# Kernel tuning notes

Hardware: AMD Instinct MI355X
Metric: run time of the kernel (lower is better)

Reference implementation:

```python
import jax, jax.numpy as jnp
import numpy as np

B, S, E, C, H = 64, 2048, 512, 512, 256


def setup_inputs() -> dict:
    key = jax.random.key(0)
    ks = jax.random.split(key, 8)
    encoder_word_embeds = jax.random.normal(ks[0], (B, S, E), dtype=jnp.float32)
    encoder_lengths = jax.random.randint(ks[1], (B,), 1, S + 1)  # lengths in [1, S]
    context_state = jax.random.normal(ks[2], (B, C), dtype=jnp.float32)
    # Learned parameters (nn.Linear style: y = x @ W.T + b)
    sw = 1.0 / np.sqrt(E)
    sc = 1.0 / np.sqrt(C)
    sh = 1.0 / np.sqrt(H)
    W_word = jax.random.uniform(ks[3], (H, E), minval=-sw, maxval=sw, dtype=jnp.float32)
    b_word = jax.random.uniform(ks[4], (H,), minval=-sw, maxval=sw, dtype=jnp.float32)
    W_ctx = jax.random.uniform(ks[5], (H, C), minval=-sc, maxval=sc, dtype=jnp.float32)
    b_ctx = jax.random.uniform(ks[6], (H,), minval=-sc, maxval=sc, dtype=jnp.float32)
    w_hidden = jax.random.uniform(ks[7], (H,), minval=-sh, maxval=sh, dtype=jnp.float32)  # hidden_layer has no bias
    return {
        "encoder_word_embeds": encoder_word_embeds,
        "encoder_lengths": encoder_lengths,
        "context_state": context_state,
        "W_word": W_word,
        "b_word": b_word,
        "W_ctx": W_ctx,
        "b_ctx": b_ctx,
        "w_hidden": w_hidden,
    }


def reference(encoder_word_embeds, encoder_lengths, context_state, W_word, b_word, W_ctx, b_ctx, w_hidden):
    seq_len = encoder_word_embeds.shape[1]
    # word mask [B, S]: positions < length
    positions = jnp.arange(seq_len)  # [S]
    mask = (positions[None, :] < encoder_lengths[:, None]).astype(jnp.float32)  # [B, S]
    # additive attention MLP
    word_feat = jnp.einsum("bse,he->bsh", encoder_word_embeds, W_word) + b_word  # [B,S,H]
    ctx_feat = context_state @ W_ctx.T + b_ctx  # [B,H]
    scores = jnp.einsum("bsh,h->bs", jnp.tanh(word_feat + ctx_feat[:, None, :]), w_hidden)  # [B,S]
    # softmax over seq, then mask and renormalize (matches original order)
    attn = jax.nn.softmax(scores, axis=1) * mask
    attn = attn / (1e-10 + attn.sum(axis=1, keepdims=True))  # [B,S]
    attention_features = jnp.einsum("bs,bse->be", attn, encoder_word_embeds)  # [B,E]
    return attention_features, attn
```

## Files before the change

kernel.cpp:

```cpp
#include <hip/hip_runtime.h>
#include <hip/hip_bf16.h>
#include <cstdint>
#include <cstddef>

#define B_  64
#define S_  2048
#define E_  512
#define C_  512
#define H_  256

using f32x4 = __attribute__((ext_vector_type(4))) float;
using s16x8 = __attribute__((ext_vector_type(8))) short;

__device__ __forceinline__ uint2 f4_to_bf4(float4 v) {
    __hip_bfloat162 lo = __float22bfloat162_rn(make_float2(v.x, v.y));
    __hip_bfloat162 hi = __float22bfloat162_rn(make_float2(v.z, v.w));
    union { __hip_bfloat162 b; unsigned u; } a, c;
    a.b = lo; c.b = hi;
    return make_uint2(a.u, c.u);
}

__global__ void prep_w(const float* __restrict__ W, unsigned short* __restrict__ Wb) {
    int i = (blockIdx.x * 256 + threadIdx.x) * 4;
    float4 v = *(const float4*)(W + i);
    uint2 o = f4_to_bf4(v);
    *(uint2*)(Wb + i) = o;
}

__global__ void prep_ctx(const float* __restrict__ ctx, const float* __restrict__ Wc,
                         const float* __restrict__ bc, const float* __restrict__ bw,
                         float* __restrict__ cb) {
    __shared__ float row[C_];
    int b = blockIdx.x, t = threadIdx.x;
    row[t] = ctx[b * C_ + t];
    row[t + 256] = ctx[b * C_ + t + 256];
    __syncthreads();
    const float4* w4 = (const float4*)(Wc + (size_t)t * C_);
    const float4* x4 = (const float4*)row;
    float acc = 0.f;
    #pragma unroll 4
    for (int c = 0; c < C_ / 4; ++c) {
        float4 w = w4[c], x = x4[c];
        acc += w.x * x.x + w.y * x.y + w.z * x.z + w.w * x.w;
    }
    cb[b * H_ + t] = acc + bc[t] + bw[t];
}

#define BM 128
#define BN 256
#define BK 64
#define LDT 72

__global__ __launch_bounds__(512) void scores_kernel(
    const float* __restrict__ A,
    const unsigned short* __restrict__ Wb,
    const float* __restrict__ cb,
    const float* __restrict__ wh,
    const int*   __restrict__ lens,
    float* __restrict__ scores)
{
    __shared__ __align__(16) unsigned short At[BM * LDT];
    __shared__ __align__(16) unsigned short Bt[BN * LDT];
    __shared__ float sblk[BM];
    int t = threadIdx.x;
    int m0 = blockIdx.x * BM;
    int b  = m0 >> 11;
    int ms = m0 & (S_ - 1);
    if (ms >= lens[b]) return;

    int w = t >> 6, lane = t & 63, quad = lane >> 4, lm = lane & 15;
    int wm = (w & 1) * 64, wn = (w >> 1) * 64;

    if (t < BM) sblk[t] = 0.f;

    f32x4 acc[4][4] = {};

    int arow = t >> 4, acol = (t & 15) * 4;
    int brow = t >> 3, bcol = (t & 7) * 8;

    for (int k0 = 0; k0 < E_; k0 += BK) {
        #pragma unroll
        for (int i = 0; i < 4; ++i) {
            int r = arow + i * 32;
            float4 v = *(const float4*)(A + (size_t)(m0 + r) * E_ + k0 + acol);
            *(uint2*)(At + r * LDT + acol) = f4_to_bf4(v);
        }
        #pragma unroll
        for (int i = 0; i < 4; ++i) {
            int r = brow + i * 64;
            uint4 v = *(const uint4*)(Wb + (size_t)r * E_ + k0 + bcol);
            *(uint4*)(Bt + r * LDT + bcol) = v;
        }
        __syncthreads();
        #pragma unroll
        for (int ks = 0; ks < 2; ++ks) {
            s16x8 af[4], bfr[4];
            #pragma unroll
            for (int i = 0; i < 4; ++i)
                af[i] = *(const s16x8*)(At + (wm + i * 16 + lm) * LDT + ks * 32 + quad * 8);
            #pragma unroll
            for (int i = 0; i < 4; ++i)
                bfr[i] = *(const s16x8*)(Bt + (wn + i * 16 + lm) * LDT + ks * 32 + quad * 8);
            #pragma unroll
            for (int mi = 0; mi < 4; ++mi)
                #pragma unroll
                for (int ni = 0; ni < 4; ++ni)
                    acc[mi][ni] = __builtin_amdgcn_mfma_f32_16x16x32_bf16(
                        af[mi], bfr[ni], acc[mi][ni], 0, 0, 0);
        }
        __syncthreads();
    }

    float wv[4], cbv[4];
    #pragma unroll
    for (int ni = 0; ni < 4; ++ni) {
        int n = wn + ni * 16 + lm;
        wv[ni]  = wh[n];
        cbv[ni] = cb[b * H_ + n];
    }
    #pragma unroll
    for (int mi = 0; mi < 4; ++mi) {
        #pragma unroll
        for (int r = 0; r < 4; ++r) {
            float p = 0.f;
            #pragma unroll
            for (int ni = 0; ni < 4; ++ni) {
                float x = acc[mi][ni][r] + cbv[ni];
                x = fminf(fmaxf(x, -15.f), 15.f);
                float e = __expf(2.f * x);
                float th = 1.f - 2.f * __builtin_amdgcn_rcpf(e + 1.f);
                p += wv[ni] * th;
            }
            #pragma unroll
            for (int off = 8; off >= 1; off >>= 1)
                p += __shfl_xor(p, off);
            if (lm == 0)
                atomicAdd(&sblk[wm + mi * 16 + quad * 4 + r], p);
        }
    }
    __syncthreads();
    if (t < BM) scores[m0 + t] = sblk[t];
}

__global__ void softmax_kernel(const int* __restrict__ lens, float* __restrict__ attn) {
    __shared__ float redm[4], redt[4];
    int b = blockIdx.x, t = threadIdx.x;
    int len = lens[b];
    float* sc = attn + (size_t)b * S_;
    float v[8];
    #pragma unroll
    for (int i = 0; i < 8; ++i) {
        int s = t + i * 256;
        v[i] = (s < len) ? sc[s] : -1e30f;
    }
    float m = -1e30f;
    #pragma unroll
    for (int i = 0; i < 8; ++i) m = fmaxf(m, v[i]);
    #pragma unroll
    for (int off = 32; off >= 1; off >>= 1) m = fmaxf(m, __shfl_xor(m, off));
    if ((t & 63) == 0) redm[t >> 6] = m;
    __syncthreads();
    m = fmaxf(fmaxf(redm[0], redm[1]), fmaxf(redm[2], redm[3]));
    float e[8]; float tm = 0.f;
    #pragma unroll
    for (int i = 0; i < 8; ++i) {
        int s = t + i * 256;
        e[i] = (s < len) ? __expf(v[i] - m) : 0.f;
        tm += e[i];
    }
    #pragma unroll
    for (int off = 32; off >= 1; off >>= 1) tm += __shfl_xor(tm, off);
    if ((t & 63) == 0) redt[t >> 6] = tm;
    __syncthreads();
    tm = redt[0] + redt[1] + redt[2] + redt[3];
    float sfac = 1.f / tm;
    #pragma unroll
    for (int i = 0; i < 8; ++i) {
        int s = t + i * 256;
        sc[s] = e[i] * sfac;
    }
}

__global__ __launch_bounds__(512) void wsum_kernel(
    const float* __restrict__ A, const float* __restrict__ attn,
    const int* __restrict__ lens, float* __restrict__ out) {
    int b = blockIdx.y;
    int len = lens[b];
    int s0 = blockIdx.x * 128;
    if (s0 >= len) return;
    int send = s0 + 128; if (send > len) send = len;
    int t  = threadIdx.x;
    int e4 = t & 127;
    int sr = t >> 7;
    const float* ap = attn + (size_t)b * S_;
    f32x4 acc = {0.f, 0.f, 0.f, 0.f};
    const float* base = A + (size_t)b * S_ * E_;
    for (int s = s0 + sr; s < send; s += 4) {
        float wgt = ap[s];
        f32x4 v = *(const f32x4*)(base + (size_t)s * E_ + e4 * 4);
        acc += wgt * v;
    }
    __shared__ f32x4 red[4][128];
    red[sr][e4] = acc;
    __syncthreads();
    if (t < 128) {
        f32x4 tot = red[0][t] + red[1][t] + red[2][t] + red[3][t];
        float* o = out + (size_t)b * E_ + t * 4;
        atomicAdd(o + 0, tot[0]);
        atomicAdd(o + 1, tot[1]);
        atomicAdd(o + 2, tot[2]);
        atomicAdd(o + 3, tot[3]);
    }
}

extern "C" void kernel_launch(void* const* d_in, const int* in_sizes, int n_in,
                              void* d_out, int out_size, void* d_ws, size_t ws_size,
                              hipStream_t stream) {
    const float* embeds = (const float*)d_in[0];
    const int*   lens   = (const int*)d_in[1];
    const float* ctx    = (const float*)d_in[2];
    const float* Ww     = (const float*)d_in[3];
    const float* bw     = (const float*)d_in[4];
    const float* Wc     = (const float*)d_in[5];
    const float* bc     = (const float*)d_in[6];
    const float* wh     = (const float*)d_in[7];
    float* out  = (float*)d_out;
    float* feat = out;
    float* attn = out + B_ * E_;

    unsigned short* Wb = (unsigned short*)d_ws;
    float* cb = (float*)((char*)d_ws + (size_t)H_ * E_ * sizeof(unsigned short));

    hipMemsetAsync(feat, 0, (size_t)B_ * E_ * sizeof(float), stream);
    prep_w<<<(H_ * E_) / 1024, 256, 0, stream>>>(Ww, Wb);
    prep_ctx<<<B_, 256, 0, stream>>>(ctx, Wc, bc, bw, cb);
    scores_kernel<<<dim3(B_ * S_ / BM), 512, 0, stream>>>(embeds, Wb, cb, wh, lens, attn);
    softmax_kernel<<<B_, 256, 0, stream>>>(lens, attn);
    wsum_kernel<<<dim3(S_ / 128, B_), 512, 0, stream>>>(embeds, attn, lens, feat);
}
```

Before: 428.7 us.

## Load weight tile via async global-to-LDS with XOR swizzle, merge prep kernels

The bf16 weight tile in the scores GEMM is now loaded with global_load_lds straight into shared memory, which skips register staging. An XOR swizzle on the column groups replaces the padded row stride to avoid bank conflicts. The two prep kernels are merged into one launch, and the memset of the output features is folded into the softmax kernel. Together these cut launch count and register pressure on the B-tile path, at the cost of relying on the async LDS load ordering being correct before the barrier.

```diff
diff --git a/kernel.cpp b/kernel.cpp
--- a/kernel.cpp
+++ b/kernel.cpp
@@ -20,30 +20,38 @@
     return make_uint2(a.u, c.u);
 }
 
-__global__ void prep_w(const float* __restrict__ W, unsigned short* __restrict__ Wb) {
-    int i = (blockIdx.x * 256 + threadIdx.x) * 4;
-    float4 v = *(const float4*)(W + i);
-    uint2 o = f4_to_bf4(v);
-    *(uint2*)(Wb + i) = o;
-}
-
-__global__ void prep_ctx(const float* __restrict__ ctx, const float* __restrict__ Wc,
-                         const float* __restrict__ bc, const float* __restrict__ bw,
-                         float* __restrict__ cb) {
+__device__ __forceinline__ void async16(const void* g, void* l) {
+    __builtin_amdgcn_global_load_lds(
+        (const __attribute__((address_space(1))) void*)g,
+        (__attribute__((address_space(3))) void*)l,
+        16, 0, 0);
+}
+
+__global__ void prep_kernel(const float* __restrict__ W, unsigned short* __restrict__ Wb,
+                            const float* __restrict__ ctx, const float* __restrict__ Wc,
+                            const float* __restrict__ bc, const float* __restrict__ bw,
+                            float* __restrict__ cb) {
     __shared__ float row[C_];
-    int b = blockIdx.x, t = threadIdx.x;
-    row[t] = ctx[b * C_ + t];
-    row[t + 256] = ctx[b * C_ + t + 256];
-    __syncthreads();
-    const float4* w4 = (const float4*)(Wc + (size_t)t * C_);
-    const float4* x4 = (const float4*)row;
-    float acc = 0.f;
-    #pragma unroll 4
-    for (int c = 0; c < C_ / 4; ++c) {
-        float4 w = w4[c], x = x4[c];
-        acc += w.x * x.x + w.y * x.y + w.z * x.z + w.w * x.w;
-    }
-    cb[b * H_ + t] = acc + bc[t] + bw[t];
+    int blk = blockIdx.x, t = threadIdx.x;
+    if (blk < 128) {
+        int i = (blk * 256 + t) * 4;
+        float4 v = *(const float4*)(W + i);
+        *(uint2*)(Wb + i) = f4_to_bf4(v);
+    } else {
+        int b = blk - 128;
+        row[t] = ctx[b * C_ + t];
+        row[t + 256] = ctx[b * C_ + t + 256];
+        __syncthreads();
+        const float4* w4 = (const float4*)(Wc + (size_t)t * C_);
+        const float4* x4 = (const float4*)row;
+        float acc = 0.f;
+        #pragma unroll 4
+        for (int c = 0; c < C_ / 4; ++c) {
+            float4 w = w4[c], x = x4[c];
+            acc += w.x * x.x + w.y * x.y + w.z * x.z + w.w * x.w;
+        }
+        cb[b * H_ + t] = acc + bc[t] + bw[t];
+    }
 }
 
 #define BM 128
@@ -60,7 +68,7 @@
     float* __restrict__ scores)
 {
     __shared__ __align__(16) unsigned short At[BM * LDT];
-    __shared__ __align__(16) unsigned short Bt[BN * LDT];
+    __shared__ __align__(16) unsigned short Bt[BN * 64];
     __shared__ float sblk[BM];
     int t = threadIdx.x;
     int m0 = blockIdx.x * BM;
@@ -76,21 +84,22 @@
     f32x4 acc[4][4] = {};
 
     int arow = t >> 4, acol = (t & 15) * 4;
-    int brow = t >> 3, bcol = (t & 7) * 8;
+    int la8 = lane >> 3, lc8 = lane & 7;
 
     for (int k0 = 0; k0 < E_; k0 += BK) {
+        #pragma unroll
+        for (int j = 0; j < 4; ++j) {
+            int r  = (w << 5) + (j << 3) + la8;
+            int cg = (lc8 ^ (r & 7)) << 3;
+            async16(Wb + (size_t)r * E_ + k0 + cg,
+                    (char*)Bt + (((w << 5) + (j << 3)) << 7));
+        }
         #pragma unroll
         for (int i = 0; i < 4; ++i) {
             int r = arow + i * 32;
             float4 v = *(const float4*)(A + (size_t)(m0 + r) * E_ + k0 + acol);
             *(uint2*)(At + r * LDT + acol) = f4_to_bf4(v);
         }
-        #pragma unroll
-        for (int i = 0; i < 4; ++i) {
-            int r = brow + i * 64;
-            uint4 v = *(const uint4*)(Wb + (size_t)r * E_ + k0 + bcol);
-            *(uint4*)(Bt + r * LDT + bcol) = v;
-        }
         __syncthreads();
         #pragma unroll
         for (int ks = 0; ks < 2; ++ks) {
@@ -99,8 +108,11 @@
             for (int i = 0; i < 4; ++i)
                 af[i] = *(const s16x8*)(At + (wm + i * 16 + lm) * LDT + ks * 32 + quad * 8);
             #pragma unroll
-            for (int i = 0; i < 4; ++i)
-                bfr[i] = *(const s16x8*)(Bt + (wn + i * 16 + lm) * LDT + ks * 32 + quad * 8);
+            for (int i = 0; i < 4; ++i) {
+                int r = wn + i * 16 + lm;
+                int c = (ks * 4 + quad) ^ (r & 7);
+                bfr[i] = *(const s16x8*)(Bt + r * 64 + c * 8);
+            }
             #pragma unroll
             for (int mi = 0; mi < 4; ++mi)
                 #pragma unroll
@@ -142,11 +154,14 @@
     if (t < BM) scores[m0 + t] = sblk[t];
 }
 
-__global__ void softmax_kernel(const int* __restrict__ lens, float* __restrict__ attn) {
+__global__ void softmax_kernel(const int* __restrict__ lens, float* __restrict__ attn,
+                               float* __restrict__ feat) {
     __shared__ float redm[4], redt[4];
     int b = blockIdx.x, t = threadIdx.x;
     int len = lens[b];
     float* sc = attn + (size_t)b * S_;
+    feat[b * E_ + t] = 0.f;
+    feat[b * E_ + 256 + t] = 0.f;
     float v[8];
     #pragma unroll
     for (int i = 0; i < 8; ++i) {
@@ -231,10 +246,8 @@
     unsigned short* Wb = (unsigned short*)d_ws;
     float* cb = (float*)((char*)d_ws + (size_t)H_ * E_ * sizeof(unsigned short));
 
-    hipMemsetAsync(feat, 0, (size_t)B_ * E_ * sizeof(float), stream);
-    prep_w<<<(H_ * E_) / 1024, 256, 0, stream>>>(Ww, Wb);
-    prep_ctx<<<B_, 256, 0, stream>>>(ctx, Wc, bc, bw, cb);
+    prep_kernel<<<192, 256, 0, stream>>>(Ww, Wb, ctx, Wc, bc, bw, cb);
     scores_kernel<<<dim3(B_ * S_ / BM), 512, 0, stream>>>(embeds, Wb, cb, wh, lens, attn);
-    softmax_kernel<<<B_, 256, 0, stream>>>(lens, attn);
+    softmax_kernel<<<B_, 256, 0, stream>>>(lens, attn, feat);
     wsum_kernel<<<dim3(S_ / 128, B_), 512, 0, stream>>>(embeds, attn, lens, feat);
 }
```

Measured after the change: 407.7 us. 1.05x faster.
